# Performance work log

Measured on AMD Instinct MI355X. Metric: run time of the kernel, lower is better.

## Reference

```python
import jax, jax.numpy as jnp
import numpy as np


def setup_inputs() -> dict:
    key = jax.random.key(0)
    k1, k2, k3, k4 = jax.random.split(key, 4)
    B, C, H, W = 16, 256, 64, 64
    OUT = 256
    x = jax.random.normal(k1, (B, C, H, W), dtype=jnp.float32)
    context = jax.random.normal(k2, (B, C, H, W), dtype=jnp.float32)
    # conv1: 1x1 Conv2d(in=C, out=OUT) -> weight [OUT, C], bias [OUT]
    w1 = jax.random.normal(k3, (OUT, C), dtype=jnp.float32) * (1.0 / np.sqrt(C))
    b1 = jax.random.normal(k4, (OUT,), dtype=jnp.float32) * 0.01
    return {"x": x, "context": context, "w1": w1, "b1": b1}


def reference(x, context, w1, b1):
    # AdaptiveAvgPool2d((1,1)) over context -> per-(b,c) scalar scale [B, C]
    scale = jnp.mean(context, axis=(2, 3))
    # grouped conv with groups=B*C and 1x1 kernels == per-channel elementwise scale
    depth_feat = x * scale[:, :, None, None]  # [B, C, H, W]
    # 1x1 pointwise conv: contract channel dim
    out = jnp.einsum("bchw,oc->bohw", depth_feat, w1) + b1[None, :, None, None]
    return out
```

## Files before the change

### kernel.cpp

```cpp
#include <hip/hip_runtime.h>
#include <hip/hip_bf16.h>


typedef __attribute__((ext_vector_type(8))) short short8;
typedef __attribute__((ext_vector_type(4))) float f32x4;

static __device__ __forceinline__ unsigned short f2bf(float f) {
    unsigned int u = __float_as_uint(f);
    unsigned int r = u + 0x7FFFu + ((u >> 16) & 1u);
    return (unsigned short)(r >> 16);
}

__global__ __launch_bounds__(256) void scale_kernel(const float* __restrict__ ctx,
                                                    float* __restrict__ scale) {
    const int bc = blockIdx.x;
    const float4* p = (const float4*)(ctx + (size_t)bc * 4096);
    const int t = threadIdx.x;
    float s = 0.f;
#pragma unroll
    for (int k = 0; k < 4; k++) {
        float4 v = p[t + k * 256];
        s += v.x + v.y + v.z + v.w;
    }
#pragma unroll
    for (int off = 32; off > 0; off >>= 1) s += __shfl_down(s, off);
    __shared__ float ws[4];
    if ((t & 63) == 0) ws[t >> 6] = s;
    __syncthreads();
    if (t == 0) scale[bc] = (ws[0] + ws[1] + ws[2] + ws[3]) * (1.0f / 4096.0f);
}

__global__ __launch_bounds__(256) void w2_kernel(const float* __restrict__ w1,
                                                 const float* __restrict__ scale,
                                                 unsigned short* __restrict__ w2) {
    const int idx = blockIdx.x * 256 + threadIdx.x;
    const int c4 = idx * 4;
    const int b = c4 >> 16;
    const int oc = c4 & 65535;
    const int c = oc & 255;
    float4 w = *(const float4*)(w1 + oc);
    float4 sc = *(const float4*)(scale + b * 256 + c);
    ushort4 r;
    r.x = f2bf(w.x * sc.x);
    r.y = f2bf(w.y * sc.y);
    r.z = f2bf(w.z * sc.z);
    r.w = f2bf(w.w * sc.w);
    *(ushort4*)(w2 + (size_t)b * 65536 + oc) = r;
}

__global__ __launch_bounds__(256) void gemm_kernel(const float* __restrict__ x,
                                                   const unsigned short* __restrict__ w2,
                                                   const float* __restrict__ b1,
                                                   float* __restrict__ out) {
    const int bid = blockIdx.x;
    const int b = bid >> 6;
    const int hw0 = (bid & 63) * 64;
    const int w = threadIdx.x >> 6;
    const int lane = threadIdx.x & 63;
    const int g = lane >> 4;
    const int lr = lane & 15;
    const int o0 = w * 64;

    const unsigned short* Aw = w2 + (size_t)b * 65536;
    const float* Xb = x + (size_t)b * (256 * 4096);

    f32x4 acc[4][4];
#pragma unroll
    for (int m = 0; m < 4; m++)
#pragma unroll
        for (int n = 0; n < 4; n++) acc[m][n] = (f32x4)(0.f);

    const float* xcol = Xb + (size_t)(g * 8) * 4096 + hw0 + lr;

#pragma unroll
    for (int ks = 0; ks < 8; ks++) {
        short8 a[4];
#pragma unroll
        for (int m = 0; m < 4; m++)
            a[m] = *(const short8*)(Aw + (o0 + m * 16 + lr) * 256 + ks * 32 + g * 8);
#pragma unroll
        for (int n = 0; n < 4; n++) {
            const float* p = xcol + (size_t)ks * 32 * 4096 + n * 16;
            short8 bf;
#pragma unroll
            for (int e = 0; e < 8; e++) bf[e] = (short)f2bf(p[(size_t)e * 4096]);
#pragma unroll
            for (int m = 0; m < 4; m++)
                acc[m][n] = __builtin_amdgcn_mfma_f32_16x16x32_bf16(a[m], bf, acc[m][n], 0, 0, 0);
        }
    }

    float* outb = out + ((size_t)b * 256) * 4096;
#pragma unroll
    for (int m = 0; m < 4; m++) {
        float bias[4];
#pragma unroll
        for (int r = 0; r < 4; r++) bias[r] = b1[o0 + m * 16 + g * 4 + r];
#pragma unroll
        for (int n = 0; n < 4; n++) {
#pragma unroll
            for (int r = 0; r < 4; r++) {
                const int row = o0 + m * 16 + g * 4 + r;
                outb[(size_t)row * 4096 + hw0 + n * 16 + lr] = acc[m][n][r] + bias[r];
            }
        }
    }
}

extern "C" void kernel_launch(void* const* d_in, const int* in_sizes, int n_in,
                              void* d_out, int out_size, void* d_ws, size_t ws_size,
                              hipStream_t stream) {
    const float* x = (const float*)d_in[0];
    const float* context = (const float*)d_in[1];
    const float* w1 = (const float*)d_in[2];
    const float* b1 = (const float*)d_in[3];
    float* out = (float*)d_out;

    float* scale = (float*)d_ws;
    unsigned short* w2 = (unsigned short*)((char*)d_ws + 16384);

    scale_kernel<<<4096, 256, 0, stream>>>(context, scale);
    w2_kernel<<<1024, 256, 0, stream>>>(w1, scale, w2);
    gemm_kernel<<<1024, 256, 0, stream>>>(x, w2, b1, out);
}
```

Measured before the change: 49.44 us.

## Stage bf16-converted X tile in LDS with swizzle, halve HW tile per block

The GEMM kernel now loads its X tile cooperatively with float4 loads, converts it to packed bf16 once, and stores it in swizzled shared memory. This replaces the per-wave strided scalar global loads and the fourfold redundant conversion, since every wave previously reloaded and converted the same X columns. B fragments are then assembled from LDS with byte-permute. The HW tile shrinks to 32 so twice as many blocks launch, with a launch-bounds occupancy hint of 6. In exchange, W2 fragments are reloaded for half as much work, and each block pays an extra barrier plus 16KB of LDS.

Result: slower. 59.13 us (+19.6%).

```diff
diff --git a/kernel.cpp b/kernel.cpp
--- a/kernel.cpp
+++ b/kernel.cpp
@@ -4,11 +4,22 @@
 
 typedef __attribute__((ext_vector_type(8))) short short8;
 typedef __attribute__((ext_vector_type(4))) float f32x4;
+typedef __attribute__((ext_vector_type(4))) unsigned int u32x4;
 
 static __device__ __forceinline__ unsigned short f2bf(float f) {
     unsigned int u = __float_as_uint(f);
     unsigned int r = u + 0x7FFFu + ((u >> 16) & 1u);
     return (unsigned short)(r >> 16);
+}
+
+static __device__ __forceinline__ unsigned int perm_b32(unsigned int a, unsigned int b,
+                                                        unsigned int sel, int half) {
+#if __has_builtin(__builtin_amdgcn_perm)
+    (void)half;
+    return __builtin_amdgcn_perm(a, b, sel);
+#else
+    return half ? ((a & 0xffff0000u) | (b >> 16)) : ((a << 16) | (b & 0xffffu));
+#endif
 }
 
 __global__ __launch_bounds__(256) void scale_kernel(const float* __restrict__ ctx,
@@ -48,15 +59,18 @@
     *(ushort4*)(w2 + (size_t)b * 65536 + oc) = r;
 }
 
-__global__ __launch_bounds__(256) void gemm_kernel(const float* __restrict__ x,
-                                                   const unsigned short* __restrict__ w2,
-                                                   const float* __restrict__ b1,
-                                                   float* __restrict__ out) {
+__global__ __launch_bounds__(256, 6) void gemm_kernel(const float* __restrict__ x,
+                                                      const unsigned short* __restrict__ w2,
+                                                      const float* __restrict__ b1,
+                                                      float* __restrict__ out) {
+    __shared__ unsigned int xl[4096];
+
     const int bid = blockIdx.x;
-    const int b = bid >> 6;
-    const int hw0 = (bid & 63) * 64;
-    const int w = threadIdx.x >> 6;
-    const int lane = threadIdx.x & 63;
+    const int b = bid >> 7;
+    const int hw0 = (bid & 127) * 32;
+    const int tid = threadIdx.x;
+    const int w = tid >> 6;
+    const int lane = tid & 63;
     const int g = lane >> 4;
     const int lr = lane & 15;
     const int o0 = w * 64;
@@ -64,13 +78,31 @@
     const unsigned short* Aw = w2 + (size_t)b * 65536;
     const float* Xb = x + (size_t)b * (256 * 4096);
 
-    f32x4 acc[4][4];
+#pragma unroll
+    for (int i = 0; i < 8; i++) {
+        const int flat = i * 256 + tid;
+        const int k = flat >> 3;
+        const int cd = (flat & 7) * 2;
+        float4 v = *(const float4*)(Xb + (size_t)k * 4096 + hw0 + cd * 2);
+        unsigned int lo = (unsigned int)f2bf(v.x) | ((unsigned int)f2bf(v.y) << 16);
+        unsigned int hi = (unsigned int)f2bf(v.z) | ((unsigned int)f2bf(v.w) << 16);
+        const int dw = k * 16 + (cd ^ (((k >> 3) & 1) << 3));
+        *(uint2*)&xl[dw] = make_uint2(lo, hi);
+    }
+    __syncthreads();
+
+    f32x4 acc[4][2];
 #pragma unroll
     for (int m = 0; m < 4; m++)
 #pragma unroll
-        for (int n = 0; n < 4; n++) acc[m][n] = (f32x4)(0.f);
+        for (int n = 0; n < 2; n++) acc[m][n] = (f32x4)(0.f);
 
-    const float* xcol = Xb + (size_t)(g * 8) * 4096 + hw0 + lr;
+    const int half = lr & 1;
+    const unsigned int sel = half ? 0x07060302u : 0x05040100u;
+    int csw[2];
+#pragma unroll
+    for (int nt = 0; nt < 2; nt++)
+        csw[nt] = ((nt * 16 + lr) >> 1) ^ ((g & 1) << 3);
 
 #pragma unroll
     for (int ks = 0; ks < 8; ks++) {
@@ -78,31 +110,33 @@
 #pragma unroll
         for (int m = 0; m < 4; m++)
             a[m] = *(const short8*)(Aw + (o0 + m * 16 + lr) * 256 + ks * 32 + g * 8);
+
 #pragma unroll
-        for (int n = 0; n < 4; n++) {
-            const float* p = xcol + (size_t)ks * 32 * 4096 + n * 16;
-            short8 bf;
+        for (int nt = 0; nt < 2; nt++) {
+            const int dwb = (ks * 32 + g * 8) * 16 + csw[nt];
+            unsigned int d[8];
 #pragma unroll
-            for (int e = 0; e < 8; e++) bf[e] = (short)f2bf(p[(size_t)e * 4096]);
+            for (int e = 0; e < 8; e++) d[e] = xl[dwb + e * 16];
+            u32x4 pv;
+#pragma unroll
+            for (int j = 0; j < 4; j++) pv[j] = perm_b32(d[2 * j + 1], d[2 * j], sel, half);
+            short8 bf = __builtin_bit_cast(short8, pv);
 #pragma unroll
             for (int m = 0; m < 4; m++)
-                acc[m][n] = __builtin_amdgcn_mfma_f32_16x16x32_bf16(a[m], bf, acc[m][n], 0, 0, 0);
+                acc[m][nt] = __builtin_amdgcn_mfma_f32_16x16x32_bf16(a[m], bf, acc[m][nt], 0, 0, 0);
         }
     }
 
-    float* outb = out + ((size_t)b * 256) * 4096;
+    float* outb = out + (size_t)b * 256 * 4096 + hw0;
 #pragma unroll
     for (int m = 0; m < 4; m++) {
-        float bias[4];
 #pragma unroll
-        for (int r = 0; r < 4; r++) bias[r] = b1[o0 + m * 16 + g * 4 + r];
+        for (int r = 0; r < 4; r++) {
+            const int row = o0 + m * 16 + g * 4 + r;
+            const float bias = b1[row];
 #pragma unroll
-        for (int n = 0; n < 4; n++) {
-#pragma unroll
-            for (int r = 0; r < 4; r++) {
-                const int row = o0 + m * 16 + g * 4 + r;
-                outb[(size_t)row * 4096 + hw0 + n * 16 + lr] = acc[m][n][r] + bias[r];
-            }
+            for (int nt = 0; nt < 2; nt++)
+                outb[(size_t)row * 4096 + nt * 16 + lr] = acc[m][nt][r] + bias;
         }
     }
 }
@@ -121,5 +155,5 @@
 
     scale_kernel<<<4096, 256, 0, stream>>>(context, scale);
     w2_kernel<<<1024, 256, 0, stream>>>(w1, scale, w2);
-    gemm_kernel<<<1024, 256, 0, stream>>>(x, w2, b1, out);
+    gemm_kernel<<<2048, 256, 0, stream>>>(x, w2, b1, out);
 }
```

## Pre-swizzle scaled weights into MFMA fragment order and retile GEMM with prefetch

Applied to the files above, without the earlier changes.

The weight-scaling kernel now writes bf16 weights directly in MFMA A-fragment order, so each lane loads its fragment with one contiguous 16-byte read. The GEMM is retiled to 32 spatial columns per block (2048 blocks), with each wave covering 128 outputs by 16 columns. X loads for the next k-step are prefetched into registers, bf16 packing uses a byte-permute, and occupancy is hinted at 4 blocks per CU. The aim is to cut strided weight loads and hide X latency. The risk is more weight traffic per block and narrower 16-wide output stores.

Result: slower. 51.52 us (+4.2%).

```diff
diff --git a/kernel.cpp b/kernel.cpp
--- a/kernel.cpp
+++ b/kernel.cpp
@@ -4,11 +4,19 @@
 
 typedef __attribute__((ext_vector_type(8))) short short8;
 typedef __attribute__((ext_vector_type(4))) float f32x4;
+typedef __attribute__((ext_vector_type(4))) unsigned int u32x4;
 
-static __device__ __forceinline__ unsigned short f2bf(float f) {
+static __device__ __forceinline__ unsigned int bfbits(float f) {
     unsigned int u = __float_as_uint(f);
-    unsigned int r = u + 0x7FFFu + ((u >> 16) & 1u);
-    return (unsigned short)(r >> 16);
+    return u + 0x7FFFu + ((u >> 16) & 1u);
+}
+
+static __device__ __forceinline__ unsigned int pkbf(float lo, float hi) {
+#if __has_builtin(__builtin_amdgcn_perm)
+    return __builtin_amdgcn_perm(bfbits(hi), bfbits(lo), 0x07060302u);
+#else
+    return (bfbits(lo) >> 16) | (bfbits(hi) & 0xffff0000u);
+#endif
 }
 
 __global__ __launch_bounds__(256) void scale_kernel(const float* __restrict__ ctx,
@@ -30,79 +38,90 @@
     if (t == 0) scale[bc] = (ws[0] + ws[1] + ws[2] + ws[3]) * (1.0f / 4096.0f);
 }
 
-__global__ __launch_bounds__(256) void w2_kernel(const float* __restrict__ w1,
-                                                 const float* __restrict__ scale,
-                                                 unsigned short* __restrict__ w2) {
-    const int idx = blockIdx.x * 256 + threadIdx.x;
-    const int c4 = idx * 4;
-    const int b = c4 >> 16;
-    const int oc = c4 & 65535;
-    const int c = oc & 255;
-    float4 w = *(const float4*)(w1 + oc);
-    float4 sc = *(const float4*)(scale + b * 256 + c);
-    ushort4 r;
-    r.x = f2bf(w.x * sc.x);
-    r.y = f2bf(w.y * sc.y);
-    r.z = f2bf(w.z * sc.z);
-    r.w = f2bf(w.w * sc.w);
-    *(ushort4*)(w2 + (size_t)b * 65536 + oc) = r;
+__global__ __launch_bounds__(256) void w2f_kernel(const float* __restrict__ w1,
+                                                  const float* __restrict__ scale,
+                                                  unsigned short* __restrict__ w2f) {
+    const int gt = blockIdx.x * 256 + threadIdx.x;
+    const int lane = gt & 63;
+    const int m16 = (gt >> 6) & 15;
+    const int ks = (gt >> 10) & 7;
+    const int b = gt >> 13;
+    const int lr = lane & 15;
+    const int g = lane >> 4;
+    const int row = m16 * 16 + lr;
+    const int c0 = ks * 32 + g * 8;
+
+    const float* wr = w1 + row * 256 + c0;
+    const float* sc = scale + b * 256 + c0;
+    float4 wv0 = *(const float4*)(wr);
+    float4 wv1 = *(const float4*)(wr + 4);
+    float4 sv0 = *(const float4*)(sc);
+    float4 sv1 = *(const float4*)(sc + 4);
+
+    u32x4 pv;
+    pv[0] = pkbf(wv0.x * sv0.x, wv0.y * sv0.y);
+    pv[1] = pkbf(wv0.z * sv0.z, wv0.w * sv0.w);
+    pv[2] = pkbf(wv1.x * sv1.x, wv1.y * sv1.y);
+    pv[3] = pkbf(wv1.z * sv1.z, wv1.w * sv1.w);
+    *(u32x4*)(w2f + (size_t)gt * 8) = pv;
 }
 
-__global__ __launch_bounds__(256) void gemm_kernel(const float* __restrict__ x,
-                                                   const unsigned short* __restrict__ w2,
-                                                   const float* __restrict__ b1,
-                                                   float* __restrict__ out) {
+__global__ __launch_bounds__(256, 4) void gemm_kernel(const float* __restrict__ x,
+                                                      const unsigned short* __restrict__ w2f,
+                                                      const float* __restrict__ b1,
+                                                      float* __restrict__ out) {
     const int bid = blockIdx.x;
-    const int b = bid >> 6;
-    const int hw0 = (bid & 63) * 64;
-    const int w = threadIdx.x >> 6;
-    const int lane = threadIdx.x & 63;
+    const int b = bid >> 7;
+    const int hw0 = (bid & 127) * 32;
+    const int tid = threadIdx.x;
+    const int w = tid >> 6;
+    const int lane = tid & 63;
     const int g = lane >> 4;
     const int lr = lane & 15;
-    const int o0 = w * 64;
+    const int o0 = (w & 1) * 128;
+    const int cw = hw0 + (w >> 1) * 16;
+    const int m16b = (w & 1) * 8;
 
-    const unsigned short* Aw = w2 + (size_t)b * 65536;
-    const float* Xb = x + (size_t)b * (256 * 4096);
+    const unsigned short* Af = w2f + (size_t)b * 65536;
+    const float* Xcol = x + (size_t)b * (256 * 4096) + cw + lr;
 
-    f32x4 acc[4][4];
+    f32x4 acc[8];
 #pragma unroll
-    for (int m = 0; m < 4; m++)
+    for (int m = 0; m < 8; m++) acc[m] = (f32x4)(0.f);
+
+    float bcur[8], bnxt[8];
 #pragma unroll
-        for (int n = 0; n < 4; n++) acc[m][n] = (f32x4)(0.f);
-
-    const float* xcol = Xb + (size_t)(g * 8) * 4096 + hw0 + lr;
+    for (int e = 0; e < 8; e++) bcur[e] = Xcol[(size_t)(g * 8 + e) * 4096];
 
 #pragma unroll
     for (int ks = 0; ks < 8; ks++) {
-        short8 a[4];
+        if (ks < 7) {
 #pragma unroll
-        for (int m = 0; m < 4; m++)
-            a[m] = *(const short8*)(Aw + (o0 + m * 16 + lr) * 256 + ks * 32 + g * 8);
+            for (int e = 0; e < 8; e++)
+                bnxt[e] = Xcol[(size_t)((ks + 1) * 32 + g * 8 + e) * 4096];
+        }
+        short8 a[8];
 #pragma unroll
-        for (int n = 0; n < 4; n++) {
-            const float* p = xcol + (size_t)ks * 32 * 4096 + n * 16;
-            short8 bf;
+        for (int m = 0; m < 8; m++)
+            a[m] = *(const short8*)(Af + ((size_t)(ks * 16 + m16b + m) * 64 + lane) * 8);
+        u32x4 pv;
 #pragma unroll
-            for (int e = 0; e < 8; e++) bf[e] = (short)f2bf(p[(size_t)e * 4096]);
+        for (int j = 0; j < 4; j++) pv[j] = pkbf(bcur[2 * j], bcur[2 * j + 1]);
+        short8 bf = __builtin_bit_cast(short8, pv);
 #pragma unroll
-            for (int m = 0; m < 4; m++)
-                acc[m][n] = __builtin_amdgcn_mfma_f32_16x16x32_bf16(a[m], bf, acc[m][n], 0, 0, 0);
-        }
+        for (int m = 0; m < 8; m++)
+            acc[m] = __builtin_amdgcn_mfma_f32_16x16x32_bf16(a[m], bf, acc[m], 0, 0, 0);
+#pragma unroll
+        for (int e = 0; e < 8; e++) bcur[e] = bnxt[e];
     }
 
-    float* outb = out + ((size_t)b * 256) * 4096;
+    float* outp = out + (size_t)b * 256 * 4096 + cw + lr;
 #pragma unroll
-    for (int m = 0; m < 4; m++) {
-        float bias[4];
+    for (int m = 0; m < 8; m++) {
 #pragma unroll
-        for (int r = 0; r < 4; r++) bias[r] = b1[o0 + m * 16 + g * 4 + r];
-#pragma unroll
-        for (int n = 0; n < 4; n++) {
-#pragma unroll
-            for (int r = 0; r < 4; r++) {
-                const int row = o0 + m * 16 + g * 4 + r;
-                outb[(size_t)row * 4096 + hw0 + n * 16 + lr] = acc[m][n][r] + bias[r];
-            }
+        for (int r = 0; r < 4; r++) {
+            const int row = o0 + m * 16 + g * 4 + r;
+            outp[(size_t)row * 4096] = acc[m][r] + b1[row];
         }
     }
 }
@@ -117,9 +136,9 @@
     float* out = (float*)d_out;
 
     float* scale = (float*)d_ws;
-    unsigned short* w2 = (unsigned short*)((char*)d_ws + 16384);
+    unsigned short* w2f = (unsigned short*)((char*)d_ws + 16384);
 
     scale_kernel<<<4096, 256, 0, stream>>>(context, scale);
-    w2_kernel<<<1024, 256, 0, stream>>>(w1, scale, w2);
-    gemm_kernel<<<1024, 256, 0, stream>>>(x, w2, b1, out);
+    w2f_kernel<<<512, 256, 0, stream>>>(w1, scale, w2f);
+    gemm_kernel<<<2048, 256, 0, stream>>>(x, w2f, b1, out);
 }
```
